# Kernel optimization log

Hardware: AMD Instinct MI355X
Metric: run time of the kernel (lower is better)

Reference implementation:

```python
import jax, jax.numpy as jnp
import numpy as np


@jax.custom_vjp
def sign_ste(x):
    return jnp.sign(x)

def _sign_ste_fwd(x):
    return jnp.sign(x), x

def _sign_ste_bwd(x, g):
    gate = (jnp.abs(x) < 1.0).astype(g.dtype)
    return (g * gate,)

sign_ste.defvjp(_sign_ste_fwd, _sign_ste_bwd)


def setup_inputs() -> dict:
    key = jax.random.key(0)
    ks = jax.random.split(key, 6)
    B, S, D_IN, D_OUT, R = 4, 4096, 4096, 4096, 128
    x = jax.random.normal(ks[0], (B, S, D_IN), dtype=jnp.float32)
    U_latent = jax.random.normal(ks[1], (D_OUT, R), dtype=jnp.float32) * 0.05
    V_latent = jax.random.normal(ks[2], (D_IN, R), dtype=jnp.float32) * 0.05
    s1 = jax.random.uniform(ks[3], (D_OUT,), dtype=jnp.float32, minval=0.01, maxval=0.1)
    s2 = jax.random.uniform(ks[4], (D_IN,), dtype=jnp.float32, minval=0.01, maxval=0.1)
    bias = jax.random.normal(ks[5], (D_OUT,), dtype=jnp.float32) * 0.02
    return {"x": x, "U_latent": U_latent, "V_latent": V_latent, "s1": s1, "s2": s2, "bias": bias}


def reference(x, U_latent, V_latent, s1, s2, bias):
    cdtype = x.dtype
    U_sign = sign_ste(U_latent.astype(cdtype))  # [d_out, r]
    V_sign = sign_ste(V_latent.astype(cdtype))  # [d_in, r]
    z = x * s2.astype(cdtype)                   # [..., d_in]
    z = z @ V_sign                               # [..., r]
    z = z @ U_sign.T                             # [..., d_out]
    z = z * s1.astype(cdtype)
    z = z + bias.astype(cdtype)
    return z
```

## Files before the change

### kernel.cpp

```cpp
#include <hip/hip_runtime.h>

typedef float f32x4 __attribute__((ext_vector_type(4)));
typedef _Float16 f16x8 __attribute__((ext_vector_type(8)));
typedef _Float16 f16x4 __attribute__((ext_vector_type(4)));

#define M_TOT 16384
#define K_IN  4096
#define R_DIM 128
#define N_OUT 4096

__device__ __forceinline__ _Float16 sign_f16(float v) {
  return v > 0.f ? (_Float16)1.f : (v < 0.f ? (_Float16)-1.f : (_Float16)0.f);
}

__global__ __launch_bounds__(256)
void k_prep(const float* __restrict__ U, const float* __restrict__ V,
            _Float16* __restrict__ VsT, _Float16* __restrict__ Us) {
  __shared__ _Float16 tl[128 * 36];
  const int t = threadIdx.x;
  const int b = blockIdx.x;
  const int k0 = b * 32;

#pragma unroll
  for (int e = 0; e < 16; ++e) {
    int idx = e * 256 + t;
    int k = idx >> 7;
    int r = idx & 127;
    tl[r * 36 + k] = sign_f16(V[(size_t)(k0 + k) * R_DIM + r]);
  }
  __syncthreads();

  {
    const int r = t >> 1;
    const int kh = (t & 1) * 16;
    f16x8 o0, o1;
#pragma unroll
    for (int j = 0; j < 8; ++j) {
      o0[j] = tl[r * 36 + kh + j];
      o1[j] = tl[r * 36 + kh + 8 + j];
    }
    *(f16x8*)(VsT + (size_t)r * K_IN + k0 + kh) = o0;
    *(f16x8*)(VsT + (size_t)r * K_IN + k0 + kh + 8) = o1;
  }

#pragma unroll
  for (int e = 0; e < 4; ++e) {
    size_t base = (size_t)b * 4096 + (size_t)e * 1024 + (size_t)t * 4;
    f32x4 u = *(const f32x4*)(U + base);
    f16x4 s;
#pragma unroll
    for (int j = 0; j < 4; ++j) s[j] = sign_f16(u[j]);
    *(f16x4*)(Us + base) = s;
  }
}

__global__ __launch_bounds__(256, 2)
void k1_z(const float* __restrict__ x, const float* __restrict__ s2,
          const _Float16* __restrict__ VsT, float* __restrict__ Z2) {
  const int t = threadIdx.x;
  const int lane = t & 63;
  const int wave = t >> 6;
  const int wid = blockIdx.x * 4 + wave;
  const int half = wid & 1;
  const int g = wid >> 1;
  const int m0 = g * 16;
  const int k0 = half * 2048;
  const int row = lane & 15;
  const int kq = (lane >> 4) * 8;

  const float* xp = x + (size_t)(m0 + row) * K_IN + k0 + kq;
  const float* sp = s2 + k0 + kq;
  const _Float16* bp = VsT + (size_t)row * K_IN + k0 + kq;

  f32x4 acc[8];
#pragma unroll
  for (int i = 0; i < 8; ++i) acc[i] = (f32x4){0.f, 0.f, 0.f, 0.f};

  f32x4 xa0 = *(const f32x4*)xp;
  f32x4 xa1 = *(const f32x4*)(xp + 4);
  f32x4 sa0 = *(const f32x4*)sp;
  f32x4 sa1 = *(const f32x4*)(sp + 4);

  for (int st = 0; st < 64; ++st) {
    f16x8 bfr[8];
#pragma unroll
    for (int nf = 0; nf < 8; ++nf)
      bfr[nf] = *(const f16x8*)(bp + (size_t)nf * 16 * K_IN + st * 32);

    f16x8 ah, al;
#pragma unroll
    for (int j = 0; j < 4; ++j) {
      float f0 = xa0[j] * sa0[j];
      float f1 = xa1[j] * sa1[j];
      _Float16 h0 = (_Float16)f0;
      _Float16 h1 = (_Float16)f1;
      ah[j] = h0;
      ah[j + 4] = h1;
      al[j] = (_Float16)(f0 - (float)h0);
      al[j + 4] = (_Float16)(f1 - (float)h1);
    }

    const int sn = (st + 1) & 63;
    xa0 = *(const f32x4*)(xp + sn * 32);
    xa1 = *(const f32x4*)(xp + sn * 32 + 4);
    sa0 = *(const f32x4*)(sp + sn * 32);
    sa1 = *(const f32x4*)(sp + sn * 32 + 4);

#pragma unroll
    for (int nf = 0; nf < 8; ++nf) {
      acc[nf] = __builtin_amdgcn_mfma_f32_16x16x32_f16(ah, bfr[nf], acc[nf], 0, 0, 0);
      acc[nf] = __builtin_amdgcn_mfma_f32_16x16x32_f16(al, bfr[nf], acc[nf], 0, 0, 0);
    }
  }

  float* Zp = Z2 + (size_t)half * M_TOT * R_DIM;
  const int rw = m0 + (lane >> 4) * 4;
#pragma unroll
  for (int nf = 0; nf < 8; ++nf) {
    const int col = nf * 16 + row;
#pragma unroll
    for (int j = 0; j < 4; ++j)
      Zp[(size_t)(rw + j) * R_DIM + col] = acc[nf][j];
  }
}

__global__ __launch_bounds__(512, 4)
void k2_out(const float* __restrict__ Z2, const _Float16* __restrict__ Us,
            const float* __restrict__ s1, const float* __restrict__ bias,
            float* __restrict__ out) {
  __shared__ _Float16 Zhi[128 * 128];
  __shared__ _Float16 Zlo[128 * 128];

  const int t = threadIdx.x;
  const int lane = t & 63;
  const int wave = t >> 6;
  const int bid = blockIdx.x;
  const int nb = bid & 31;
  const int mb = bid >> 5;
  const int m0 = mb * 128, n0 = nb * 128;
  const int wm = wave & 1, wn = wave >> 1;

  f16x8 bf[4][2];
#pragma unroll
  for (int ks = 0; ks < 4; ++ks)
#pragma unroll
    for (int nf = 0; nf < 2; ++nf) {
      const int n = n0 + wn * 32 + nf * 16 + (lane & 15);
      bf[ks][nf] = *(const f16x8*)(Us + (size_t)n * R_DIM + ks * 32 + (lane >> 4) * 8);
    }

  {
    const int sr = t >> 2;
    const int skf = (t & 3) * 32;
    const float* za = Z2 + (size_t)(m0 + sr) * R_DIM + skf;
    const float* zb = za + (size_t)M_TOT * R_DIM;
    const int swr = (sr & 7) << 4;
#pragma unroll
    for (int q = 0; q < 4; ++q) {
      f32x4 a0 = *(const f32x4*)(za + q * 8);
      f32x4 a1 = *(const f32x4*)(za + q * 8 + 4);
      f32x4 b0 = *(const f32x4*)(zb + q * 8);
      f32x4 b1 = *(const f32x4*)(zb + q * 8 + 4);
      f16x8 h, l;
#pragma unroll
      for (int j = 0; j < 4; ++j) {
        float f0 = a0[j] + b0[j];
        float f1 = a1[j] + b1[j];
        _Float16 h0 = (_Float16)f0, h1 = (_Float16)f1;
        h[j] = h0;
        h[j + 4] = h1;
        l[j] = (_Float16)(f0 - (float)h0);
        l[j + 4] = (_Float16)(f1 - (float)h1);
      }
      const int off = sr * 256 + ((((t & 3) * 64) + q * 16) ^ swr);
      *(f16x8*)((char*)Zhi + off) = h;
      *(f16x8*)((char*)Zlo + off) = l;
    }
  }
  __syncthreads();

  f32x4 acc[4][2] = {};
  const int rsw = (lane & 7) << 4;
  const int kg = (lane >> 4) * 16;
#pragma unroll
  for (int mf = 0; mf < 4; ++mf) {
    const int r = wm * 64 + mf * 16 + (lane & 15);
    const int rbase = r * 256;
#pragma unroll
    for (int ks = 0; ks < 4; ++ks) {
      const int kb = ks * 64 + kg;
      f16x8 ah = *(const f16x8*)((const char*)Zhi + rbase + (kb ^ rsw));
      f16x8 al = *(const f16x8*)((const char*)Zlo + rbase + (kb ^ rsw));
#pragma unroll
      for (int nf = 0; nf < 2; ++nf) {
        acc[mf][nf] = __builtin_amdgcn_mfma_f32_16x16x32_f16(ah, bf[ks][nf], acc[mf][nf], 0, 0, 0);
        acc[mf][nf] = __builtin_amdgcn_mfma_f32_16x16x32_f16(al, bf[ks][nf], acc[mf][nf], 0, 0, 0);
      }
    }
  }

#pragma unroll
  for (int nf = 0; nf < 2; ++nf) {
    const int col = n0 + wn * 32 + nf * 16 + (lane & 15);
    const float sv = s1[col];
    const float bv = bias[col];
#pragma unroll
    for (int mf = 0; mf < 4; ++mf) {
      const int row2 = m0 + wm * 64 + mf * 16 + (lane >> 4) * 4;
#pragma unroll
      for (int j = 0; j < 4; ++j)
        out[(size_t)(row2 + j) * N_OUT + col] = acc[mf][nf][j] * sv + bv;
    }
  }
}

extern "C" void kernel_launch(void* const* d_in, const int* in_sizes, int n_in,
                              void* d_out, int out_size, void* d_ws, size_t ws_size,
                              hipStream_t stream) {
  const float* x    = (const float*)d_in[0];
  const float* U    = (const float*)d_in[1];
  const float* V    = (const float*)d_in[2];
  const float* s1   = (const float*)d_in[3];
  const float* s2   = (const float*)d_in[4];
  const float* bias = (const float*)d_in[5];
  float* out = (float*)d_out;

  _Float16* VsT = (_Float16*)d_ws;
  _Float16* Us  = VsT + (size_t)R_DIM * K_IN;
  float*    Z2  = (float*)(Us + (size_t)N_OUT * R_DIM);

  k_prep<<<dim3(128), dim3(256), 0, stream>>>(U, V, VsT, Us);
  k1_z<<<dim3(512), dim3(256), 0, stream>>>(x, s2, VsT, Z2);
  k2_out<<<dim3(4096), dim3(512), 0, stream>>>(Z2, Us, s1, bias, out);
}
```

Baseline: 637.3 us.

## Restructure both GEMM stages with LDS staging, swizzled fp16 split Z and async loads

Result: faster. 524.5 us (-17.7%).

```diff
diff --git a/kernel.cpp b/kernel.cpp
--- a/kernel.cpp
+++ b/kernel.cpp
@@ -2,7 +2,7 @@
 
 typedef float f32x4 __attribute__((ext_vector_type(4)));
 typedef _Float16 f16x8 __attribute__((ext_vector_type(8)));
-typedef _Float16 f16x4 __attribute__((ext_vector_type(4)));
+typedef __fp16 fp16x2 __attribute__((ext_vector_type(2)));
 
 #define M_TOT 16384
 #define K_IN  4096
@@ -13,186 +13,222 @@
   return v > 0.f ? (_Float16)1.f : (v < 0.f ? (_Float16)-1.f : (_Float16)0.f);
 }
 
+__device__ __forceinline__ void cvt8v(f32x4 a, f32x4 b, f16x8& h, f16x8& l) {
+#pragma unroll
+  for (int j = 0; j < 2; ++j) {
+    fp16x2 h0 = __builtin_amdgcn_cvt_pkrtz(a[2 * j], a[2 * j + 1]);
+    fp16x2 h1 = __builtin_amdgcn_cvt_pkrtz(b[2 * j], b[2 * j + 1]);
+    fp16x2 l0 = __builtin_amdgcn_cvt_pkrtz(a[2 * j] - (float)h0[0], a[2 * j + 1] - (float)h0[1]);
+    fp16x2 l1 = __builtin_amdgcn_cvt_pkrtz(b[2 * j] - (float)h1[0], b[2 * j + 1] - (float)h1[1]);
+    h[2 * j] = (_Float16)h0[0]; h[2 * j + 1] = (_Float16)h0[1];
+    h[4 + 2 * j] = (_Float16)h1[0]; h[5 + 2 * j] = (_Float16)h1[1];
+    l[2 * j] = (_Float16)l0[0]; l[2 * j + 1] = (_Float16)l0[1];
+    l[4 + 2 * j] = (_Float16)l1[0]; l[5 + 2 * j] = (_Float16)l1[1];
+  }
+}
+
+__device__ __forceinline__ void gload16(const void* g, void* l) {
+  __builtin_amdgcn_global_load_lds((const __attribute__((address_space(1))) unsigned int*)g,
+                                   (__attribute__((address_space(3))) unsigned int*)l, 16, 0, 0);
+}
+
 __global__ __launch_bounds__(256)
 void k_prep(const float* __restrict__ U, const float* __restrict__ V,
-            _Float16* __restrict__ VsT, _Float16* __restrict__ Us) {
-  __shared__ _Float16 tl[128 * 36];
+            _Float16* __restrict__ VsT_sw, _Float16* __restrict__ Us) {
+  __shared__ _Float16 tl[128 * 72];
   const int t = threadIdx.x;
   const int b = blockIdx.x;
-  const int k0 = b * 32;
-
-#pragma unroll
-  for (int e = 0; e < 16; ++e) {
-    int idx = e * 256 + t;
-    int k = idx >> 7;
-    int r = idx & 127;
-    tl[r * 36 + k] = sign_f16(V[(size_t)(k0 + k) * R_DIM + r]);
-  }
-  __syncthreads();
 
   {
-    const int r = t >> 1;
-    const int kh = (t & 1) * 16;
-    f16x8 o0, o1;
-#pragma unroll
-    for (int j = 0; j < 8; ++j) {
-      o0[j] = tl[r * 36 + kh + j];
-      o1[j] = tl[r * 36 + kh + 8 + j];
-    }
-    *(f16x8*)(VsT + (size_t)r * K_IN + k0 + kh) = o0;
-    *(f16x8*)(VsT + (size_t)r * K_IN + k0 + kh + 8) = o1;
-  }
-
-#pragma unroll
-  for (int e = 0; e < 4; ++e) {
-    size_t base = (size_t)b * 4096 + (size_t)e * 1024 + (size_t)t * 4;
-    f32x4 u = *(const f32x4*)(U + base);
-    f16x4 s;
-#pragma unroll
-    for (int j = 0; j < 4; ++j) s[j] = sign_f16(u[j]);
-    *(f16x4*)(Us + base) = s;
-  }
-}
-
-__global__ __launch_bounds__(256, 2)
+    size_t base = (size_t)b * 2048 + (size_t)t * 8;
+    f32x4 u0 = *(const f32x4*)(U + base);
+    f32x4 u1 = *(const f32x4*)(U + base + 4);
+    f16x8 s;
+#pragma unroll
+    for (int j = 0; j < 4; ++j) { s[j] = sign_f16(u0[j]); s[j + 4] = sign_f16(u1[j]); }
+    *(f16x8*)(Us + base) = s;
+  }
+
+  if (b < 64) {
+#pragma unroll
+    for (int it = 0; it < 8; ++it) {
+      int idx4 = it * 256 + t;
+      int kl = idx4 >> 5;
+      int r4 = (idx4 & 31) * 4;
+      f32x4 v = *(const f32x4*)(V + (size_t)(b * 64 + kl) * R_DIM + r4);
+#pragma unroll
+      for (int j = 0; j < 4; ++j) tl[(r4 + j) * 72 + kl] = sign_f16(v[j]);
+    }
+    __syncthreads();
+#pragma unroll
+    for (int c = 0; c < 4; ++c) {
+      int off = t * 64 + c * 16;
+      int r = off >> 7;
+      int cB = (off & 127) ^ ((r & 7) << 4);
+      f16x8 o = *(const f16x8*)(tl + r * 72 + (cB >> 1));
+      *(f16x8*)((char*)VsT_sw + (size_t)b * 16384 + off) = o;
+    }
+  }
+}
+
+__global__ __launch_bounds__(256, 3)
 void k1_z(const float* __restrict__ x, const float* __restrict__ s2,
-          const _Float16* __restrict__ VsT, float* __restrict__ Z2) {
+          const _Float16* __restrict__ VsT_sw,
+          _Float16* __restrict__ Zswh, _Float16* __restrict__ Zswl) {
+  __shared__ char smem[49152];
   const int t = threadIdx.x;
   const int lane = t & 63;
   const int wave = t >> 6;
-  const int wid = blockIdx.x * 4 + wave;
-  const int half = wid & 1;
-  const int g = wid >> 1;
-  const int m0 = g * 16;
-  const int k0 = half * 2048;
-  const int row = lane & 15;
-  const int kq = (lane >> 4) * 8;
-
-  const float* xp = x + (size_t)(m0 + row) * K_IN + k0 + kq;
-  const float* sp = s2 + k0 + kq;
-  const _Float16* bp = VsT + (size_t)row * K_IN + k0 + kq;
-
-  f32x4 acc[8];
-#pragma unroll
-  for (int i = 0; i < 8; ++i) acc[i] = (f32x4){0.f, 0.f, 0.f, 0.f};
-
-  f32x4 xa0 = *(const f32x4*)xp;
-  f32x4 xa1 = *(const f32x4*)(xp + 4);
-  f32x4 sa0 = *(const f32x4*)sp;
-  f32x4 sa1 = *(const f32x4*)(sp + 4);
-
-  for (int st = 0; st < 64; ++st) {
-    f16x8 bfr[8];
-#pragma unroll
-    for (int nf = 0; nf < 8; ++nf)
-      bfr[nf] = *(const f16x8*)(bp + (size_t)nf * 16 * K_IN + st * 32);
-
-    f16x8 ah, al;
-#pragma unroll
-    for (int j = 0; j < 4; ++j) {
-      float f0 = xa0[j] * sa0[j];
-      float f1 = xa1[j] * sa1[j];
-      _Float16 h0 = (_Float16)f0;
-      _Float16 h1 = (_Float16)f1;
-      ah[j] = h0;
-      ah[j + 4] = h1;
-      al[j] = (_Float16)(f0 - (float)h0);
-      al[j + 4] = (_Float16)(f1 - (float)h1);
-    }
-
-    const int sn = (st + 1) & 63;
-    xa0 = *(const f32x4*)(xp + sn * 32);
-    xa1 = *(const f32x4*)(xp + sn * 32 + 4);
-    sa0 = *(const f32x4*)(sp + sn * 32);
-    sa1 = *(const f32x4*)(sp + sn * 32 + 4);
-
-#pragma unroll
-    for (int nf = 0; nf < 8; ++nf) {
-      acc[nf] = __builtin_amdgcn_mfma_f32_16x16x32_f16(ah, bfr[nf], acc[nf], 0, 0, 0);
-      acc[nf] = __builtin_amdgcn_mfma_f32_16x16x32_f16(al, bfr[nf], acc[nf], 0, 0, 0);
-    }
-  }
-
-  float* Zp = Z2 + (size_t)half * M_TOT * R_DIM;
-  const int rw = m0 + (lane >> 4) * 4;
-#pragma unroll
-  for (int nf = 0; nf < 8; ++nf) {
-    const int col = nf * 16 + row;
+  const int m0 = blockIdx.x * 32;
+
+  const int srow = t >> 3;
+  const int scol = (t & 7) * 8;
+  const float* xrow = x + (size_t)(m0 + srow) * K_IN + scol;
+  const int aoff = srow * 128 + (((t & 7) * 16) ^ ((srow & 7) << 4));
+
+  const int wr = wave & 1, wc = wave >> 1;
+  const int arow = wr * 16 + (lane & 15);
+  const int abyte = arow * 128;
+  const int asw = (arow & 7) << 4;
+  const int kq16 = (lane >> 4) * 16;
+  int brow[4], bsw[4];
+#pragma unroll
+  for (int nf = 0; nf < 4; ++nf) {
+    brow[nf] = wc * 64 + nf * 16 + (lane & 15);
+    bsw[nf] = (brow[nf] & 7) << 4;
+  }
+
+  f32x4 acc[4];
+#pragma unroll
+  for (int i = 0; i < 4; ++i) acc[i] = (f32x4){0.f, 0.f, 0.f, 0.f};
+
+  {
+    f32x4 a = *(const f32x4*)xrow;
+    f32x4 bql = *(const f32x4*)(xrow + 4);
+    f32x4 sa = *(const f32x4*)(s2 + scol);
+    f32x4 sb = *(const f32x4*)(s2 + scol + 4);
+    f16x8 h, l;
+    cvt8v(a * sa, bql * sb, h, l);
+    *(f16x8*)(smem + aoff) = h;
+    *(f16x8*)(smem + 4096 + aoff) = l;
+#pragma unroll
+    for (int q = 0; q < 4; ++q)
+      gload16((const char*)VsT_sw + (size_t)wave * 1024 + q * 4096 + lane * 16,
+              smem + 16384 + wave * 1024 + q * 4096);
+  }
+  __syncthreads();
+
+  f32x4 xn0 = *(const f32x4*)(xrow + 64);
+  f32x4 xn1 = *(const f32x4*)(xrow + 68);
+  f32x4 sn0 = *(const f32x4*)(s2 + 64 + scol);
+  f32x4 sn1 = *(const f32x4*)(s2 + 64 + scol + 4);
+
+  for (int kt = 0; kt < 64; ++kt) {
+    const int cur = kt & 1, nxt = cur ^ 1;
+    if (kt < 63) {
+#pragma unroll
+      for (int q = 0; q < 4; ++q)
+        gload16((const char*)VsT_sw + (size_t)(kt + 1) * 16384 + wave * 1024 + q * 4096 + lane * 16,
+                smem + 16384 + nxt * 16384 + wave * 1024 + q * 4096);
+      f16x8 h, l;
+      cvt8v(xn0 * sn0, xn1 * sn1, h, l);
+      *(f16x8*)(smem + nxt * 8192 + aoff) = h;
+      *(f16x8*)(smem + nxt * 8192 + 4096 + aoff) = l;
+      if (kt < 62) {
+        xn0 = *(const f32x4*)(xrow + (kt + 2) * 64);
+        xn1 = *(const f32x4*)(xrow + (kt + 2) * 64 + 4);
+        sn0 = *(const f32x4*)(s2 + (kt + 2) * 64 + scol);
+        sn1 = *(const f32x4*)(s2 + (kt + 2) * 64 + scol + 4);
+      }
+    }
+#pragma unroll
+    for (int kk = 0; kk < 2; ++kk) {
+      const int cb = kk * 64 + kq16;
+      f16x8 ah = *(const f16x8*)(smem + cur * 8192 + abyte + (cb ^ asw));
+      f16x8 al = *(const f16x8*)(smem + cur * 8192 + 4096 + abyte + (cb ^ asw));
+#pragma unroll
+      for (int nf = 0; nf < 4; ++nf) {
+        f16x8 bfv = *(const f16x8*)(smem + 16384 + cur * 16384 + brow[nf] * 128 + (cb ^ bsw[nf]));
+        acc[nf] = __builtin_amdgcn_mfma_f32_16x16x32_f16(ah, bfv, acc[nf], 0, 0, 0);
+        acc[nf] = __builtin_amdgcn_mfma_f32_16x16x32_f16(al, bfv, acc[nf], 0, 0, 0);
+      }
+    }
+    __syncthreads();
+  }
+
+  float* ZT = (float*)smem;
+#pragma unroll
+  for (int nf = 0; nf < 4; ++nf)
 #pragma unroll
     for (int j = 0; j < 4; ++j)
-      Zp[(size_t)(rw + j) * R_DIM + col] = acc[nf][j];
-  }
-}
-
-__global__ __launch_bounds__(512, 4)
-void k2_out(const float* __restrict__ Z2, const _Float16* __restrict__ Us,
-            const float* __restrict__ s1, const float* __restrict__ bias,
-            float* __restrict__ out) {
-  __shared__ _Float16 Zhi[128 * 128];
-  __shared__ _Float16 Zlo[128 * 128];
-
+      ZT[(wr * 16 + (lane >> 4) * 4 + j) * 132 + wc * 64 + nf * 16 + (lane & 15)] = acc[nf][j];
+  __syncthreads();
+  {
+    const int lr = t >> 3;
+    const int c0 = (t & 7) * 16;
+    f32x4 v0 = *(const f32x4*)(ZT + lr * 132 + c0);
+    f32x4 v1 = *(const f32x4*)(ZT + lr * 132 + c0 + 4);
+    f32x4 v2 = *(const f32x4*)(ZT + lr * 132 + c0 + 8);
+    f32x4 v3 = *(const f32x4*)(ZT + lr * 132 + c0 + 12);
+    f16x8 h0, l0, h1, l1;
+    cvt8v(v0, v1, h0, l0);
+    cvt8v(v2, v3, h1, l1);
+    const int m = m0 + lr;
+    const int sw = (lr & 7) << 4;
+    char* ph = (char*)Zswh + (size_t)m * 256;
+    char* pl = (char*)Zswl + (size_t)m * 256;
+    *(f16x8*)(ph + ((c0 * 2) ^ sw)) = h0;
+    *(f16x8*)(ph + ((c0 * 2 + 16) ^ sw)) = h1;
+    *(f16x8*)(pl + ((c0 * 2) ^ sw)) = l0;
+    *(f16x8*)(pl + ((c0 * 2 + 16) ^ sw)) = l1;
+  }
+}
+
+__global__ __launch_bounds__(256, 4)
+void k2_out(const _Float16* __restrict__ Zswh, const _Float16* __restrict__ Zswl,
+            const _Float16* __restrict__ Us, const float* __restrict__ s1,
+            const float* __restrict__ bias, float* __restrict__ out) {
+  __shared__ char smem[32768];
   const int t = threadIdx.x;
   const int lane = t & 63;
   const int wave = t >> 6;
   const int bid = blockIdx.x;
   const int nb = bid & 31;
   const int mb = bid >> 5;
-  const int m0 = mb * 128, n0 = nb * 128;
+  const int m0 = mb * 64, n0 = nb * 128;
   const int wm = wave & 1, wn = wave >> 1;
 
-  f16x8 bf[4][2];
+  f16x8 bf[4][4];
 #pragma unroll
   for (int ks = 0; ks < 4; ++ks)
 #pragma unroll
-    for (int nf = 0; nf < 2; ++nf) {
-      const int n = n0 + wn * 32 + nf * 16 + (lane & 15);
+    for (int nf = 0; nf < 4; ++nf) {
+      const int n = n0 + wn * 64 + nf * 16 + (lane & 15);
       bf[ks][nf] = *(const f16x8*)(Us + (size_t)n * R_DIM + ks * 32 + (lane >> 4) * 8);
     }
 
-  {
-    const int sr = t >> 2;
-    const int skf = (t & 3) * 32;
-    const float* za = Z2 + (size_t)(m0 + sr) * R_DIM + skf;
-    const float* zb = za + (size_t)M_TOT * R_DIM;
-    const int swr = (sr & 7) << 4;
-#pragma unroll
-    for (int q = 0; q < 4; ++q) {
-      f32x4 a0 = *(const f32x4*)(za + q * 8);
-      f32x4 a1 = *(const f32x4*)(za + q * 8 + 4);
-      f32x4 b0 = *(const f32x4*)(zb + q * 8);
-      f32x4 b1 = *(const f32x4*)(zb + q * 8 + 4);
-      f16x8 h, l;
-#pragma unroll
-      for (int j = 0; j < 4; ++j) {
-        float f0 = a0[j] + b0[j];
-        float f1 = a1[j] + b1[j];
-        _Float16 h0 = (_Float16)f0, h1 = (_Float16)f1;
-        h[j] = h0;
-        h[j + 4] = h1;
-        l[j] = (_Float16)(f0 - (float)h0);
-        l[j + 4] = (_Float16)(f1 - (float)h1);
-      }
-      const int off = sr * 256 + ((((t & 3) * 64) + q * 16) ^ swr);
-      *(f16x8*)((char*)Zhi + off) = h;
-      *(f16x8*)((char*)Zlo + off) = l;
-    }
+  const char* gh = (const char*)Zswh + (size_t)m0 * 256;
+  const char* gl = (const char*)Zswl + (size_t)m0 * 256;
+#pragma unroll
+  for (int q = 0; q < 4; ++q) {
+    gload16(gh + wave * 1024 + q * 4096 + lane * 16, smem + wave * 1024 + q * 4096);
+    gload16(gl + wave * 1024 + q * 4096 + lane * 16, smem + 16384 + wave * 1024 + q * 4096);
   }
   __syncthreads();
 
-  f32x4 acc[4][2] = {};
-  const int rsw = (lane & 7) << 4;
-  const int kg = (lane >> 4) * 16;
-#pragma unroll
-  for (int mf = 0; mf < 4; ++mf) {
-    const int r = wm * 64 + mf * 16 + (lane & 15);
-    const int rbase = r * 256;
+  f32x4 acc[2][4] = {};
+  const int kq = (lane >> 4) * 16;
+#pragma unroll
+  for (int mf = 0; mf < 2; ++mf) {
+    const int lr = wm * 32 + mf * 16 + (lane & 15);
+    const int sw = (lr & 7) << 4;
 #pragma unroll
     for (int ks = 0; ks < 4; ++ks) {
-      const int kb = ks * 64 + kg;
-      f16x8 ah = *(const f16x8*)((const char*)Zhi + rbase + (kb ^ rsw));
-      f16x8 al = *(const f16x8*)((const char*)Zlo + rbase + (kb ^ rsw));
-#pragma unroll
-      for (int nf = 0; nf < 2; ++nf) {
+      const int cb = (ks * 64 + kq) ^ sw;
+      f16x8 ah = *(const f16x8*)(smem + lr * 256 + cb);
+      f16x8 al = *(const f16x8*)(smem + 16384 + lr * 256 + cb);
+#pragma unroll
+      for (int nf = 0; nf < 4; ++nf) {
         acc[mf][nf] = __builtin_amdgcn_mfma_f32_16x16x32_f16(ah, bf[ks][nf], acc[mf][nf], 0, 0, 0);
         acc[mf][nf] = __builtin_amdgcn_mfma_f32_16x16x32_f16(al, bf[ks][nf], acc[mf][nf], 0, 0, 0);
       }
@@ -200,16 +236,16 @@
   }
 
 #pragma unroll
-  for (int nf = 0; nf < 2; ++nf) {
-    const int col = n0 + wn * 32 + nf * 16 + (lane & 15);
+  for (int nf = 0; nf < 4; ++nf) {
+    const int col = n0 + wn * 64 + nf * 16 + (lane & 15);
     const float sv = s1[col];
     const float bv = bias[col];
 #pragma unroll
-    for (int mf = 0; mf < 4; ++mf) {
-      const int row2 = m0 + wm * 64 + mf * 16 + (lane >> 4) * 4;
+    for (int mf = 0; mf < 2; ++mf) {
+      const int row = m0 + wm * 32 + mf * 16 + (lane >> 4) * 4;
 #pragma unroll
       for (int j = 0; j < 4; ++j)
-        out[(size_t)(row2 + j) * N_OUT + col] = acc[mf][nf][j] * sv + bv;
+        out[(size_t)(row + j) * N_OUT + col] = acc[mf][nf][j] * sv + bv;
     }
   }
 }
@@ -225,11 +261,13 @@
   const float* bias = (const float*)d_in[5];
   float* out = (float*)d_out;
 
-  _Float16* VsT = (_Float16*)d_ws;
-  _Float16* Us  = VsT + (size_t)R_DIM * K_IN;
-  float*    Z2  = (float*)(Us + (size_t)N_OUT * R_DIM);
-
-  k_prep<<<dim3(128), dim3(256), 0, stream>>>(U, V, VsT, Us);
-  k1_z<<<dim3(512), dim3(256), 0, stream>>>(x, s2, VsT, Z2);
-  k2_out<<<dim3(4096), dim3(512), 0, stream>>>(Z2, Us, s1, bias, out);
-}
+  char* w = (char*)d_ws;
+  _Float16* VsT_sw = (_Float16*)(w);
+  _Float16* Us     = (_Float16*)(w + (1 << 20));
+  _Float16* Zswh   = (_Float16*)(w + (2 << 20));
+  _Float16* Zswl   = (_Float16*)(w + (6 << 20));
+
+  k_prep<<<dim3(256), dim3(256), 0, stream>>>(U, V, VsT_sw, Us);
+  k1_z<<<dim3(512), dim3(256), 0, stream>>>(x, s2, VsT_sw, Zswh, Zswl);
+  k2_out<<<dim3(8192), dim3(256), 0, stream>>>(Zswh, Zswl, Us, s1, bias, out);
+}
```
